# Kernel optimization log

Hardware: AMD Instinct MI355X
Metric: run time of the kernel (lower is better)

Reference implementation:

```python
import jax, jax.numpy as jnp
import numpy as np

ROWS, COLS, K = 8192, 8192, 16


def setup_inputs() -> dict:
    key = jax.random.key(0)
    x = jax.random.normal(key, (ROWS, COLS), dtype=jnp.float32)
    codebook = jnp.linspace(-3.0, 3.0, K, dtype=jnp.float32)  # uniform codebook, sorted
    return {"x": x, "codebook": codebook}


def reference(x, codebook):
    # Nearest-codeword quantization (faithful to the per-scalar argmin over |x - c|),
    # implemented O(log K) per element via searchsorted on the sorted uniform codebook
    # instead of materializing an [ROWS, COLS, K] distance tensor.
    k = codebook.shape[0]
    idx = jnp.searchsorted(codebook, x)           # in [0, K]
    lo = jnp.clip(idx - 1, 0, k - 1)
    hi = jnp.clip(idx, 0, k - 1)
    c_lo = codebook[lo]
    c_hi = codebook[hi]
    # tie-break toward the lower codeword (first minimum, like a sequential argmin scan)
    pick_lo = jnp.abs(x - c_lo) <= jnp.abs(x - c_hi)
    return jnp.where(pick_lo, c_lo, c_hi)
```

## Files before the change

kernel.cpp:

```cpp
#include <hip/hip_runtime.h>

#define KWORDS 16

__device__ __forceinline__ float quant_one(float v, const float* __restrict__ c,
                                           float c0, float inv_step) {
    float f = (v - c0) * inv_step;
    int i = (int)floorf(f + 0.5f);
    i = i < 0 ? 0 : (i > KWORDS - 1 ? KWORDS - 1 : i);
    int im = i > 0 ? i - 1 : 0;
    int ip = i < KWORDS - 1 ? i + 1 : KWORDS - 1;
    float ci = c[i];
    float cm = c[im];
    float cp = c[ip];
    float di = fabsf(v - ci);
    float dm = fabsf(v - cm);
    float dp = fabsf(v - cp);
    float r = ci;
    float dbest = di;
    if (dm <= dbest) { r = cm; dbest = dm; }
    if (dp < dbest)  { r = cp; }
    return r;
}

__global__ __launch_bounds__(256) void QuantizerUniformLayer_78975858639646_kernel(
    const float4* __restrict__ x, const float* __restrict__ cb,
    float4* __restrict__ out, int nvec,
    const float* __restrict__ x_tail, float* __restrict__ out_tail, int rem)
{
    __shared__ float c[KWORDS];
    if (threadIdx.x < KWORDS) c[threadIdx.x] = cb[threadIdx.x];
    __syncthreads();

    const float c0 = c[0];
    const float inv_step = (float)(KWORDS - 1) / (c[KWORDS - 1] - c[0]);

    const int stride = gridDim.x * blockDim.x;
    for (int idx = blockIdx.x * blockDim.x + threadIdx.x; idx < nvec; idx += stride) {
        float4 v = x[idx];
        float4 r;
        r.x = quant_one(v.x, c, c0, inv_step);
        r.y = quant_one(v.y, c, c0, inv_step);
        r.z = quant_one(v.z, c, c0, inv_step);
        r.w = quant_one(v.w, c, c0, inv_step);
        out[idx] = r;
    }

    if (blockIdx.x == 0 && (int)threadIdx.x < rem) {
        float v = x_tail[threadIdx.x];
        out_tail[threadIdx.x] = quant_one(v, c, c0, inv_step);
    }
}

extern "C" void kernel_launch(void* const* d_in, const int* in_sizes, int n_in,
                              void* d_out, int out_size, void* d_ws, size_t ws_size,
                              hipStream_t stream) {
    const float* x  = (const float*)d_in[0];
    const float* cb = (const float*)d_in[1];
    float* out = (float*)d_out;

    const int n    = in_sizes[0];
    const int nvec = n / 4;
    const int rem  = n - nvec * 4;

    const int block = 256;
    const int grid  = 8192;

    QuantizerUniformLayer_78975858639646_kernel<<<grid, block, 0, stream>>>(
        (const float4*)x, cb, (float4*)out, nvec,
        x + (size_t)nvec * 4, out + (size_t)nvec * 4, rem);
}
```

Before: 432.6 us.

## Batch eight vector loads per thread with nontemporal access and exact grid

Replaces the grid-stride loop with a fixed mapping where each thread issues eight independent 16-byte loads up front, then quantizes and stores them. Loads and stores use nontemporal builtins to avoid polluting caches in this streaming kernel. The grid is sized exactly to the data instead of a fixed 8192 blocks. This raises memory-level parallelism per thread at the cost of more registers.

```diff
diff --git a/kernel.cpp b/kernel.cpp
--- a/kernel.cpp
+++ b/kernel.cpp
@@ -1,6 +1,10 @@
 #include <hip/hip_runtime.h>
 
 #define KWORDS 16
+#define BLOCK  256
+#define VPT    8
+
+typedef float vfloat4 __attribute__((ext_vector_type(4)));
 
 __device__ __forceinline__ float quant_one(float v, const float* __restrict__ c,
                                            float c0, float inv_step) {
@@ -22,9 +26,19 @@
     return r;
 }
 
-__global__ __launch_bounds__(256) void QuantizerUniformLayer_78975858639646_kernel(
-    const float4* __restrict__ x, const float* __restrict__ cb,
-    float4* __restrict__ out, int nvec,
+__device__ __forceinline__ vfloat4 quant_vec(vfloat4 v, const float* __restrict__ c,
+                                             float c0, float inv_step) {
+    vfloat4 r;
+    r.x = quant_one(v.x, c, c0, inv_step);
+    r.y = quant_one(v.y, c, c0, inv_step);
+    r.z = quant_one(v.z, c, c0, inv_step);
+    r.w = quant_one(v.w, c, c0, inv_step);
+    return r;
+}
+
+__global__ __launch_bounds__(BLOCK) void QuantizerUniformLayer_78975858639646_kernel(
+    const vfloat4* __restrict__ x, const float* __restrict__ cb,
+    vfloat4* __restrict__ out, int nvec,
     const float* __restrict__ x_tail, float* __restrict__ out_tail, int rem)
 {
     __shared__ float c[KWORDS];
@@ -32,17 +46,30 @@
     __syncthreads();
 
     const float c0 = c[0];
-    const float inv_step = (float)(KWORDS - 1) / (c[KWORDS - 1] - c[0]);
+    const float inv_step = (float)(KWORDS - 1) / (c[KWORDS - 1] - c0);
 
-    const int stride = gridDim.x * blockDim.x;
-    for (int idx = blockIdx.x * blockDim.x + threadIdx.x; idx < nvec; idx += stride) {
-        float4 v = x[idx];
-        float4 r;
-        r.x = quant_one(v.x, c, c0, inv_step);
-        r.y = quant_one(v.y, c, c0, inv_step);
-        r.z = quant_one(v.z, c, c0, inv_step);
-        r.w = quant_one(v.w, c, c0, inv_step);
-        out[idx] = r;
+    const int base = blockIdx.x * (BLOCK * VPT) + threadIdx.x;
+
+    if (base + (VPT - 1) * BLOCK < nvec) {
+        vfloat4 v[VPT];
+#pragma unroll
+        for (int j = 0; j < VPT; ++j)
+            v[j] = __builtin_nontemporal_load(&x[base + j * BLOCK]);
+#pragma unroll
+        for (int j = 0; j < VPT; ++j) {
+            vfloat4 r = quant_vec(v[j], c, c0, inv_step);
+            __builtin_nontemporal_store(r, &out[base + j * BLOCK]);
+        }
+    } else {
+#pragma unroll
+        for (int j = 0; j < VPT; ++j) {
+            int idx = base + j * BLOCK;
+            if (idx < nvec) {
+                vfloat4 v = __builtin_nontemporal_load(&x[idx]);
+                vfloat4 r = quant_vec(v, c, c0, inv_step);
+                __builtin_nontemporal_store(r, &out[idx]);
+            }
+        }
     }
 
     if (blockIdx.x == 0 && (int)threadIdx.x < rem) {
@@ -62,10 +89,9 @@
     const int nvec = n / 4;
     const int rem  = n - nvec * 4;
 
-    const int block = 256;
-    const int grid  = 8192;
+    const int grid = (nvec + BLOCK * VPT - 1) / (BLOCK * VPT);
 
-    QuantizerUniformLayer_78975858639646_kernel<<<grid, block, 0, stream>>>(
-        (const float4*)x, cb, (float4*)out, nvec,
+    QuantizerUniformLayer_78975858639646_kernel<<<(grid > 0 ? grid : 1), BLOCK, 0, stream>>>(
+        (const vfloat4*)x, cb, (vfloat4*)out, nvec,
         x + (size_t)nvec * 4, out + (size_t)nvec * 4, rem);
 }
```

Result: faster. 414.2 us (-4.3%).
